# Kernel optimization log

Measured on AMD Instinct MI355X. Metric: run time of the kernel, lower is better.

Reference implementation:

```python
import jax, jax.numpy as jnp
import numpy as np

NUM_BITS = 8
QMIN = -(2.0 ** (NUM_BITS - 1)) + 1.0   # -127
QMAX = 2.0 ** (NUM_BITS - 1) - 1.0      # 127
RUN_MIN, RUN_MAX = -1.0, 1.0            # eval-mode running_min/running_max buffers
KERNEL, STRIDE, PAD = 3, 1, 1

# input scale (concrete, from running stats): scale = max(|min|,|max|)/qmax, snapped to power of 2
_scale_in = max(max(abs(RUN_MAX), abs(RUN_MIN)) / QMAX, 1e-8)
INPUT_SCALE = float(2.0 ** np.round(np.log2(_scale_in)))  # 2^-7


def _ste_quant(x, scale):
    """shift (x/scale), clamp to [QMIN,QMAX], round; straight-through grad = 1/scale."""
    xs = x / scale
    return xs + jax.lax.stop_gradient(jnp.round(jnp.clip(xs, QMIN, QMAX)) - xs)


def _weight_scale(w):
    s = jnp.maximum(jnp.maximum(jnp.abs(jnp.max(w)), jnp.abs(jnp.min(w))) / QMAX, 1e-8)
    return 2.0 ** jnp.round(jnp.log2(s))


def _adder2d(qx, qw):
    """AdderNet SAD conv: out[n,f,i,j] = -sum_{c,kh,kw} |patch - w|."""
    N = qx.shape[0]
    Cout = qw.shape[0]
    patches = jax.lax.conv_general_dilated_patches(
        qx, (KERNEL, KERNEL), (STRIDE, STRIDE), [(PAD, PAD), (PAD, PAD)])
    _, K, Ho, Wo = patches.shape            # K = Cin*k*k, channel-major like OIHW reshape
    pr = patches.reshape(N, K, Ho * Wo)
    wf = qw.reshape(Cout, K)

    def per_out(wk):                         # wk: [K]
        return -jnp.sum(jnp.abs(pr - wk[None, :, None]), axis=1)  # [N, Ho*Wo]

    out = jax.lax.map(jax.checkpoint(per_out), wf)   # [Cout, N, Ho*Wo], sequential over Cout
    return jnp.transpose(out, (1, 0, 2)).reshape(N, Cout, Ho, Wo)


def reference(x, weight):
    # quantize input (eval mode, running stats scale = 2^-7)
    qx = _ste_quant(x, INPUT_SCALE)
    # quantize weight at its own power-of-2 scale (scale_index < 0 branch)
    s_w = jax.lax.stop_gradient(_weight_scale(weight))
    qw = _ste_quant(weight, s_w)
    # integer-domain SAD convolution
    q_out = _adder2d(qx, qw)
    # dequantize: round, clamp to int32 range, shift right by |scale_index| (== * INPUT_SCALE);
    # straight-through grad = INPUT_SCALE
    ys = q_out * INPUT_SCALE
    deq = jnp.clip(jnp.round(q_out), -2.0 ** 31 + 1, 2.0 ** 31 - 1) * INPUT_SCALE
    return ys + jax.lax.stop_gradient(deq - ys)


def setup_inputs() -> dict:
    key = jax.random.key(0)
    kx, kw = jax.random.split(key)
    x = jax.random.normal(kx, (16, 32, 128, 128), dtype=jnp.float32)
    weight = jax.random.normal(kw, (32, 32, 3, 3), dtype=jnp.float32)
    return {"x": x, "weight": weight}
```

## Files before the change

### kernel.cpp

```cpp
#include <hip/hip_runtime.h>
#include <stdint.h>

#define INPUT_SCALE 0.0078125f

__device__ __forceinline__ uint32_t sadu8(uint32_t a, uint32_t b, uint32_t c) {
#if __has_builtin(__builtin_amdgcn_sad_u8)
    return __builtin_amdgcn_sad_u8(a, b, c);
#else
    uint32_t d;
    asm("v_sad_u8 %0, %1, %2, %3" : "=v"(d) : "v"(a), "v"(b), "v"(c));
    return d;
#endif
}

__device__ __forceinline__ uint32_t qbyte(float x) {
    float v = fminf(fmaxf(x * 128.0f, -127.0f), 127.0f);
    return (uint32_t)((int)rintf(v) + 128);
}

__global__ __launch_bounds__(256) void quant_weight(const float* __restrict__ w,
                                                    uint32_t* __restrict__ qwp) {
    __shared__ float red[256];
    __shared__ float s_inv;
    int tid = threadIdx.x;
    float m = 0.0f;
    for (int i = tid; i < 9216; i += 256) m = fmaxf(m, fabsf(w[i]));
    red[tid] = m;
    __syncthreads();
    for (int s = 128; s > 0; s >>= 1) {
        if (tid < s) red[tid] = fmaxf(red[tid], red[tid + s]);
        __syncthreads();
    }
    if (tid == 0) {
        float s = fmaxf(red[0] / 127.0f, 1e-8f);
        int e; float fr = frexpf(s, &e);
        int k = (fr >= 0.70710678118654752f) ? e : e - 1;
        s_inv = exp2f((float)(-k));
    }
    __syncthreads();
    float inv = s_inv;
    int u = blockIdx.x * 256 + tid;
    {
        int t = u >> 8;
        int rem = u & 255;
        int f = rem >> 3, cg = rem & 7;
        int kh = t / 3, kw = t - kh * 3;
        uint32_t pk = 0;
        #pragma unroll
        for (int b = 0; b < 4; ++b) {
            int c = cg * 4 + b;
            float v = w[((f * 32 + c) * 3 + kh) * 3 + kw] * inv;
            v = fminf(fmaxf(v, -127.0f), 127.0f);
            pk |= ((uint32_t)((int)rintf(v) + 128) & 0xFFu) << (8 * b);
        }
        qwp[u] = pk;
    }
}

#define LSTRIDE 12
__global__ __launch_bounds__(256, 8) void adder_conv_fused(const float* __restrict__ x,
                                                           const uint32_t* __restrict__ qwp,
                                                           float* __restrict__ out) {
    __shared__ __align__(16) uint32_t sx[6 * 18 * LSTRIDE];
    int tid = threadIdx.x;
    int b = ((blockIdx.x & 7) << 9) + (blockIdx.x >> 3);
    int n = b >> 8;
    int rem = b & 255;
    int h0 = (rem >> 3) * 4, w0 = (rem & 7) * 16;

    for (int q = tid; q < 864; q += 256) {
        int cg = q / 108;
        int pixel = q - cg * 108;
        int r = pixel / 18, cc = pixel - r * 18;
        int gh = h0 - 1 + r, gw = w0 - 1 + cc;
        uint32_t pk = 0x80808080u;
        if ((unsigned)gh < 128u && (unsigned)gw < 128u) {
            const float* base = x + (((size_t)n * 32 + cg * 4) * 128 + gh) * 128 + gw;
            pk = qbyte(base[0])
               | (qbyte(base[16384]) << 8)
               | (qbyte(base[32768]) << 16)
               | (qbyte(base[49152]) << 24);
        }
        sx[pixel * LSTRIDE + cg] = pk;
    }
    __syncthreads();

    int fg = __builtin_amdgcn_readfirstlane(tid >> 6);
    int px = tid & 63;
    int r = px >> 4;
    int c = px & 15;

    uint32_t acc[8];
    #pragma unroll
    for (int f = 0; f < 8; ++f) acc[f] = 0u;

    int lb = (r * 18 + c) * LSTRIDE;
    #pragma unroll 1
    for (int kh = 0; kh < 3; ++kh) {
        #pragma unroll 1
        for (int kw = 0; kw < 3; ++kw) {
            const uint4* p = (const uint4*)(sx + lb + (kh * 18 + kw) * LSTRIDE);
            uint4 x0 = p[0];
            uint4 x1 = p[1];
            const uint32_t* wt = qwp + ((kh * 3 + kw) * 32 + fg * 8) * 8;
            #pragma unroll
            for (int f = 0; f < 8; ++f) {
                const uint4* wp = (const uint4*)(wt + f * 8);
                uint4 wv0 = wp[0], wv1 = wp[1];
                uint32_t a = acc[f];
                a = sadu8(x0.x, wv0.x, a);
                a = sadu8(x0.y, wv0.y, a);
                a = sadu8(x0.z, wv0.z, a);
                a = sadu8(x0.w, wv0.w, a);
                a = sadu8(x1.x, wv1.x, a);
                a = sadu8(x1.y, wv1.y, a);
                a = sadu8(x1.z, wv1.z, a);
                a = sadu8(x1.w, wv1.w, a);
                acc[f] = a;
            }
        }
    }

    size_t obase = (((size_t)n * 32 + fg * 8) * 16384) + (size_t)(h0 + r) * 128 + (w0 + c);
    #pragma unroll
    for (int f = 0; f < 8; ++f) {
        out[obase + (size_t)f * 16384] = -(float)acc[f] * INPUT_SCALE;
    }
}

extern "C" void kernel_launch(void* const* d_in, const int* in_sizes, int n_in,
                              void* d_out, int out_size, void* d_ws, size_t ws_size,
                              hipStream_t stream) {
    const float* x = (const float*)d_in[0];
    const float* w = (const float*)d_in[1];
    float* out = (float*)d_out;

    uint32_t* qwp = (uint32_t*)d_ws;

    quant_weight<<<9, 256, 0, stream>>>(w, qwp);
    adder_conv_fused<<<4096, 256, 0, stream>>>(x, qwp, out);
}
```

Baseline: 41.95 us.

## Enlarge spatial tile to 16x16 with 4 rows per thread and stage weights in LDS

New measurement: 44.96 us. 1.07x slower.

```diff
diff --git a/kernel.cpp b/kernel.cpp
--- a/kernel.cpp
+++ b/kernel.cpp
@@ -58,19 +58,23 @@
 }
 
 #define LSTRIDE 12
-__global__ __launch_bounds__(256, 8) void adder_conv_fused(const float* __restrict__ x,
+__global__ __launch_bounds__(256, 4) void adder_conv_fused(const float* __restrict__ x,
                                                            const uint32_t* __restrict__ qwp,
                                                            float* __restrict__ out) {
-    __shared__ __align__(16) uint32_t sx[6 * 18 * LSTRIDE];
+    __shared__ __align__(16) uint32_t sx[18 * 18 * LSTRIDE];
+    __shared__ __align__(16) uint32_t swl[2304];
     int tid = threadIdx.x;
-    int b = ((blockIdx.x & 7) << 9) + (blockIdx.x >> 3);
-    int n = b >> 8;
-    int rem = b & 255;
-    int h0 = (rem >> 3) * 4, w0 = (rem & 7) * 16;
+    int b = ((blockIdx.x & 7) << 7) + (blockIdx.x >> 3);
+    int n = b >> 6;
+    int rem = b & 63;
+    int h0 = (rem >> 3) * 16, w0 = (rem & 7) * 16;
 
-    for (int q = tid; q < 864; q += 256) {
-        int cg = q / 108;
-        int pixel = q - cg * 108;
+    for (int i = tid; i < 576; i += 256)
+        ((uint4*)swl)[i] = ((const uint4*)qwp)[i];
+
+    for (int q = tid; q < 2592; q += 256) {
+        int cg = q / 324;
+        int pixel = q - cg * 324;
         int r = pixel / 18, cc = pixel - r * 18;
         int gh = h0 - 1 + r, gw = w0 - 1 + cc;
         uint32_t pk = 0x80808080u;
@@ -86,45 +90,54 @@
     __syncthreads();
 
     int fg = __builtin_amdgcn_readfirstlane(tid >> 6);
-    int px = tid & 63;
-    int r = px >> 4;
-    int c = px & 15;
+    int lane = tid & 63;
+    int c  = lane & 15;
+    int r0 = lane >> 4;
 
-    uint32_t acc[8];
+    uint32_t acc[4][8];
     #pragma unroll
-    for (int f = 0; f < 8; ++f) acc[f] = 0u;
+    for (int j = 0; j < 4; ++j)
+        #pragma unroll
+        for (int f = 0; f < 8; ++f) acc[j][f] = 0u;
 
-    int lb = (r * 18 + c) * LSTRIDE;
     #pragma unroll 1
-    for (int kh = 0; kh < 3; ++kh) {
-        #pragma unroll 1
-        for (int kw = 0; kw < 3; ++kw) {
-            const uint4* p = (const uint4*)(sx + lb + (kh * 18 + kw) * LSTRIDE);
-            uint4 x0 = p[0];
-            uint4 x1 = p[1];
-            const uint32_t* wt = qwp + ((kh * 3 + kw) * 32 + fg * 8) * 8;
+    for (int t = 0; t < 9; ++t) {
+        int kh = t / 3, kw = t - kh * 3;
+        uint4 px[4][2];
+        #pragma unroll
+        for (int j = 0; j < 4; ++j) {
+            const uint4* p = (const uint4*)(sx + ((r0 + 4 * j + kh) * 18 + (c + kw)) * LSTRIDE);
+            px[j][0] = p[0];
+            px[j][1] = p[1];
+        }
+        const uint32_t* wt = swl + (t * 32 + fg * 8) * 8;
+        #pragma unroll
+        for (int f = 0; f < 8; ++f) {
+            const uint4* wp = (const uint4*)(wt + f * 8);
+            uint4 wv0 = wp[0], wv1 = wp[1];
             #pragma unroll
-            for (int f = 0; f < 8; ++f) {
-                const uint4* wp = (const uint4*)(wt + f * 8);
-                uint4 wv0 = wp[0], wv1 = wp[1];
-                uint32_t a = acc[f];
-                a = sadu8(x0.x, wv0.x, a);
-                a = sadu8(x0.y, wv0.y, a);
-                a = sadu8(x0.z, wv0.z, a);
-                a = sadu8(x0.w, wv0.w, a);
-                a = sadu8(x1.x, wv1.x, a);
-                a = sadu8(x1.y, wv1.y, a);
-                a = sadu8(x1.z, wv1.z, a);
-                a = sadu8(x1.w, wv1.w, a);
-                acc[f] = a;
+            for (int j = 0; j < 4; ++j) {
+                uint32_t a = acc[j][f];
+                a = sadu8(px[j][0].x, wv0.x, a);
+                a = sadu8(px[j][0].y, wv0.y, a);
+                a = sadu8(px[j][0].z, wv0.z, a);
+                a = sadu8(px[j][0].w, wv0.w, a);
+                a = sadu8(px[j][1].x, wv1.x, a);
+                a = sadu8(px[j][1].y, wv1.y, a);
+                a = sadu8(px[j][1].z, wv1.z, a);
+                a = sadu8(px[j][1].w, wv1.w, a);
+                acc[j][f] = a;
             }
         }
     }
 
-    size_t obase = (((size_t)n * 32 + fg * 8) * 16384) + (size_t)(h0 + r) * 128 + (w0 + c);
     #pragma unroll
     for (int f = 0; f < 8; ++f) {
-        out[obase + (size_t)f * 16384] = -(float)acc[f] * INPUT_SCALE;
+        size_t obase = ((size_t)(n * 32 + fg * 8 + f) * 16384) + (size_t)h0 * 128 + (w0 + c);
+        #pragma unroll
+        for (int j = 0; j < 4; ++j) {
+            out[obase + (size_t)(r0 + 4 * j) * 128] = -(float)acc[j][f] * INPUT_SCALE;
+        }
     }
 }
 
@@ -138,5 +151,5 @@
     uint32_t* qwp = (uint32_t*)d_ws;
 
     quant_weight<<<9, 256, 0, stream>>>(w, qwp);
-    adder_conv_fused<<<4096, 256, 0, stream>>>(x, qwp, out);
+    adder_conv_fused<<<1024, 256, 0, stream>>>(x, qwp, out);
 }
```
